# Kernel optimization log

Measured on AMD Instinct MI355X. Metric: run time of the kernel, lower is better.

Reference implementation:

```python
import jax, jax.numpy as jnp
import numpy as np

B, SQ, SK, DQ, DKV, DH, DV = 8, 2048, 2048, 1024, 1024, 1024, 1024


def setup_inputs() -> dict:
    ks = jax.random.split(jax.random.key(0), 10)
    q = jax.random.normal(ks[0], (B, SQ, DQ), dtype=jnp.float32)
    k = jax.random.normal(ks[1], (B, SK, DKV), dtype=jnp.float32)
    v = jax.random.normal(ks[2], (B, SK, DKV), dtype=jnp.float32)
    mask = jax.random.randint(ks[3], (B, SK), 0, 2).astype(jnp.bool_)
    s = 1.0 / np.sqrt(DQ)
    Wq = jax.random.normal(ks[4], (DQ, DH), dtype=jnp.float32) * s
    bq = jnp.zeros((DH,), dtype=jnp.float32)
    Wk = jax.random.normal(ks[5], (DKV, DH), dtype=jnp.float32) * s
    bk = jnp.zeros((DH,), dtype=jnp.float32)
    Wv = jax.random.normal(ks[6], (DKV, DV), dtype=jnp.float32) * s
    bv = jnp.zeros((DV,), dtype=jnp.float32)
    return {"q": q, "k": k, "v": v, "mask": mask,
            "Wq": Wq, "bq": bq, "Wk": Wk, "bk": bk, "Wv": Wv, "bv": bv}


def reference(q, k, v, mask, Wq, bq, Wk, bk, Wv, bv):
    # Linear projections
    Qp = q @ Wq + bq                       # [B, SQ, DH]
    Kp = k @ Wk + bk                       # [B, SK, DH]
    Vp = jnp.tanh(v @ Wv + bv)             # [B, SK, DV] (value has Tanh)
    # Scores; NOTE: original adds the *bool* mask, i.e. +0/+1, not -inf masking
    qk = jnp.einsum('bqd,bkd->bqk', Qp, Kp)
    qk = qk + mask[:, None, :].astype(qk.dtype)   # broadcast of mask.unsqueeze(1)
    attn = jax.nn.softmax(qk, axis=-1)
    out = jnp.einsum('bqk,bkd->bqd', attn, Vp)    # [B, SQ, DV]
    return out
```

## Files before the change

### kernel.cpp

```cpp
#include <hip/hip_runtime.h>
#include <math.h>

#define BB 8
#define SQL 2048
#define SKL 2048
#define DD 1024

typedef __attribute__((ext_vector_type(8))) short bf16x8;
typedef __attribute__((ext_vector_type(4))) float f32x4;
typedef __attribute__((ext_vector_type(4))) unsigned short us4;
typedef unsigned short u16;

__device__ __forceinline__ u16 f2bf(float f) {
    unsigned u = __float_as_uint(f);
    u += 0x7fffu + ((u >> 16) & 1u);
    return (u16)(u >> 16);
}
__device__ __forceinline__ float bf2f(u16 h) {
    return __uint_as_float((unsigned)h << 16);
}

__global__ __launch_bounds__(256)
void split3(const float* __restrict__ in, u16* __restrict__ oh,
            u16* __restrict__ ol, long n4) {
    long i = (long)blockIdx.x * 256 + threadIdx.x;
    if (i >= n4) return;
    float4 v = ((const float4*)in)[i];
    us4 h, l;
    h.x = f2bf(v.x); l.x = f2bf(v.x - bf2f(h.x));
    h.y = f2bf(v.y); l.y = f2bf(v.y - bf2f(h.y));
    h.z = f2bf(v.z); l.z = f2bf(v.z - bf2f(h.z));
    h.w = f2bf(v.w); l.w = f2bf(v.w - bf2f(h.w));
    ((us4*)oh)[i] = h;
    ((us4*)ol)[i] = l;
}

__global__ __launch_bounds__(256)
void splitT3(const float* __restrict__ W, u16* __restrict__ WhT,
             u16* __restrict__ WlT) {
    __shared__ float t[32][33];
    const int n0 = blockIdx.x * 32, k0 = blockIdx.y * 32;
    const int tx = threadIdx.x & 31, ty = threadIdx.x >> 5;
#pragma unroll
    for (int r = 0; r < 32; r += 8)
        t[ty + r][tx] = W[(long)(k0 + ty + r) * DD + n0 + tx];
    __syncthreads();
#pragma unroll
    for (int r = 0; r < 32; r += 8) {
        float x = t[tx][ty + r];
        u16 h = f2bf(x);
        WhT[(long)(n0 + ty + r) * DD + k0 + tx] = h;
        WlT[(long)(n0 + ty + r) * DD + k0 + tx] = f2bf(x - bf2f(h));
    }
}

#define GLL(gp, lp) __builtin_amdgcn_global_load_lds( \
    (const __attribute__((address_space(1))) void*)(gp), \
    (__attribute__((address_space(3))) void*)(lp), 16, 0, 0)

__global__ __launch_bounds__(512, 2)
void gemm3(const u16* __restrict__ Ah, const u16* __restrict__ Al,
           const u16* __restrict__ Bh, const u16* __restrict__ Bl,
           int lda, int ldb, int K, long sA, long sB,
           const float* __restrict__ bias, const int* __restrict__ mask, int sM,
           float* __restrict__ Cf, u16* __restrict__ C1, u16* __restrict__ C2,
           long sC, int ldc, int mode)
{
    __shared__ u16 L[65536];

    const int z = blockIdx.z;
    const long zA = (long)z * sA, zB = (long)z * sB;
    const int tid = threadIdx.x, lane = tid & 63, wave = tid >> 6;
    const int wm = wave >> 2, wn = wave & 3;
    const int l15 = lane & 15, lq = lane >> 4;
    const long row0 = (long)blockIdx.y * 256, col0 = (long)blockIdx.x * 256;

    const int pl = tid >> 8;
    const int c = tid & 255;
    const int srow = c >> 2;
    const int qg = (c & 3) ^ ((srow >> 1) & 3);
    const u16* sAp = (pl ? Al : Ah) + zA + qg * 8;
    const u16* sBp = (pl ? Bl : Bh) + zB + qg * 8;
    int ofA[4], ofB[4];
#pragma unroll
    for (int p = 0; p < 4; p++) {
        ofA[p] = (int)((row0 + p * 64 + srow) * (long)lda);
        ofB[p] = (int)((col0 + p * 64 + srow) * (long)ldb);
    }
    const int dst = tid * 8;

#define STB(p, kk, bb) GLL(sBp + ofB[p] + (kk), L + (bb) + 16384 + (p) * 4096 + dst)
#define STA(p, kk, bb) GLL(sAp + ofA[p] + (kk), L + (bb) + (p) * 4096 + dst)

    int aoff[8], boff[4];
#pragma unroll
    for (int i = 0; i < 8; i++) {
        int r = wm * 128 + i * 16 + l15;
        aoff[i] = (r >> 6) * 4096 + (r & 63) * 32 + ((lq ^ ((r >> 1) & 3)) * 8);
    }
#pragma unroll
    for (int j = 0; j < 4; j++) {
        int r = wn * 64 + j * 16 + l15;
        boff[j] = 16384 + (r >> 6) * 4096 + (r & 63) * 32 + ((lq ^ ((r >> 1) & 3)) * 8);
    }

    f32x4 acc[8][4];
#pragma unroll
    for (int i = 0; i < 8; i++)
#pragma unroll
        for (int j = 0; j < 4; j++)
#pragma unroll
            for (int e = 0; e < 4; e++) acc[i][j][e] = 0.f;

#define PHASE(mh) do { \
    bf16x8 xh[4], xl[4], yh[4], yl[4]; \
    _Pragma("unroll") \
    for (int ii = 0; ii < 4; ii++) { \
        xh[ii] = *(const bf16x8*)(L + bo + aoff[(mh) * 4 + ii]); \
        xl[ii] = *(const bf16x8*)(L + bo + aoff[(mh) * 4 + ii] + 2048); \
    } \
    _Pragma("unroll") \
    for (int j = 0; j < 4; j++) { \
        yh[j] = *(const bf16x8*)(L + bo + boff[j]); \
        yl[j] = *(const bf16x8*)(L + bo + boff[j] + 2048); \
    } \
    __builtin_amdgcn_s_setprio(1); \
    _Pragma("unroll") \
    for (int ii = 0; ii < 4; ii++) { \
        _Pragma("unroll") \
        for (int j = 0; j < 4; j++) { \
            f32x4 t_ = acc[(mh) * 4 + ii][j]; \
            t_ = __builtin_amdgcn_mfma_f32_16x16x32_bf16(xh[ii], yh[j], t_, 0, 0, 0); \
            t_ = __builtin_amdgcn_mfma_f32_16x16x32_bf16(xh[ii], yl[j], t_, 0, 0, 0); \
            t_ = __builtin_amdgcn_mfma_f32_16x16x32_bf16(xl[ii], yh[j], t_, 0, 0, 0); \
            acc[(mh) * 4 + ii][j] = t_; \
        } \
    } \
    __builtin_amdgcn_s_setprio(0); \
} while (0)

    const int NT = K >> 5;
    STB(0, 0, 0); STB(1, 0, 0); STB(2, 0, 0); STB(3, 0, 0);
    STA(0, 0, 0); STA(2, 0, 0); STA(1, 0, 0); STA(3, 0, 0);

    for (int t = 0; t < NT; ++t) {
        const int bo = (t & 1) << 15;
        const int bn = bo ^ 32768;
        const int kn = (t + 1) << 5;
        const bool pf = (t + 1) < NT;

        asm volatile("s_waitcnt vmcnt(2)" ::: "memory");
        __builtin_amdgcn_s_barrier();
        __builtin_amdgcn_sched_barrier(0);
        if (pf) { STB(0, kn, bn); STB(1, kn, bn); STB(2, kn, bn); STB(3, kn, bn); }
        PHASE(0);

        if (pf) asm volatile("s_waitcnt vmcnt(4)" ::: "memory");
        else    asm volatile("s_waitcnt vmcnt(0)" ::: "memory");
        __builtin_amdgcn_s_barrier();
        __builtin_amdgcn_sched_barrier(0);
        if (pf) { STA(0, kn, bn); STA(2, kn, bn); STA(1, kn, bn); STA(3, kn, bn); }
        PHASE(1);
    }
#undef PHASE
#undef STA
#undef STB

    const long zc = (long)z * sC;
#pragma unroll
    for (int i = 0; i < 8; i++) {
#pragma unroll
        for (int j = 0; j < 4; j++) {
            const long col = col0 + wn * 64 + j * 16 + l15;
            const long rbase = row0 + wm * 128 + i * 16 + lq * 4;
            if (mode == 0 || mode == 3) {
                const float madd = (mode == 3) ? (float)mask[(long)z * sM + col] : 0.f;
#pragma unroll
                for (int r = 0; r < 4; r++)
                    Cf[zc + (rbase + r) * (long)ldc + col] = acc[i][j][r] + madd;
            } else if (mode == 1) {
                const float bv = bias[col];
#pragma unroll
                for (int r = 0; r < 4; r++) {
                    float val = acc[i][j][r] + bv;
                    u16 h = f2bf(val);
                    C1[zc + (rbase + r) * (long)ldc + col] = h;
                    C2[zc + (rbase + r) * (long)ldc + col] = f2bf(val - bf2f(h));
                }
            } else {
                const float bv = bias[col];
                us4 o;
                o.x = f2bf(tanhf(acc[i][j][0] + bv));
                o.y = f2bf(tanhf(acc[i][j][1] + bv));
                o.z = f2bf(tanhf(acc[i][j][2] + bv));
                o.w = f2bf(tanhf(acc[i][j][3] + bv));
                *(us4*)(C1 + zc + col * (long)ldc + rbase) = o;
            }
        }
    }
}

__global__ __launch_bounds__(256, 2)
void gemm1(const u16* __restrict__ A, const u16* __restrict__ B,
           float* __restrict__ C, int lda, int ldb, int K,
           long sA, long sB, long sC, int ldc)
{
    __shared__ u16 As[4096], Bs[4096];

    const int z = blockIdx.z;
    const long zA = (long)z * sA, zB = (long)z * sB;
    const int tid = threadIdx.x, lane = tid & 63, wave = tid >> 6;
    const int wm = (wave & 1) * 64, wn = (wave >> 1) * 64;
    const int l15 = lane & 15, lq = lane >> 4;
    const long row0 = (long)blockIdx.y * 128, col0 = (long)blockIdx.x * 128;

    long offA[2], offB[2]; int lds[2];
#pragma unroll
    for (int it = 0; it < 2; it++) {
        int c = tid + it * 256, row = c >> 2;
        int qg = (c & 3) ^ ((row >> 1) & 3);
        offA[it] = (row0 + row) * (long)lda + qg * 8;
        offB[it] = (col0 + row) * (long)ldb + qg * 8;
        lds[it] = c * 8;
    }
    int aoff[4], boff[4];
#pragma unroll
    for (int i = 0; i < 4; i++) {
        int r = wm + i * 16 + l15;
        aoff[i] = r * 32 + ((lq ^ ((r >> 1) & 3)) * 8);
    }
#pragma unroll
    for (int j = 0; j < 4; j++) {
        int r = wn + j * 16 + l15;
        boff[j] = r * 32 + ((lq ^ ((r >> 1) & 3)) * 8);
    }

    f32x4 acc[4][4];
#pragma unroll
    for (int i = 0; i < 4; i++)
#pragma unroll
        for (int j = 0; j < 4; j++)
#pragma unroll
            for (int e = 0; e < 4; e++) acc[i][j][e] = 0.f;

    for (int k0 = 0; k0 < K; k0 += 32) {
#pragma unroll
        for (int it = 0; it < 2; it++) {
            GLL(A + zA + offA[it] + k0, As + lds[it]);
            GLL(B + zB + offB[it] + k0, Bs + lds[it]);
        }
        __syncthreads();
        bf16x8 af[4], bf[4];
#pragma unroll
        for (int i = 0; i < 4; i++) af[i] = *(const bf16x8*)(As + aoff[i]);
#pragma unroll
        for (int j = 0; j < 4; j++) bf[j] = *(const bf16x8*)(Bs + boff[j]);
#pragma unroll
        for (int i = 0; i < 4; i++)
#pragma unroll
            for (int j = 0; j < 4; j++)
                acc[i][j] = __builtin_amdgcn_mfma_f32_16x16x32_bf16(af[i], bf[j], acc[i][j], 0, 0, 0);
        __syncthreads();
    }

    const long zc = (long)z * sC;
#pragma unroll
    for (int i = 0; i < 4; i++)
#pragma unroll
        for (int j = 0; j < 4; j++) {
            const long col = col0 + wn + j * 16 + l15;
            const long rbase = row0 + wm + i * 16 + lq * 4;
#pragma unroll
            for (int r = 0; r < 4; r++)
                C[zc + (rbase + r) * (long)ldc + col] = acc[i][j][r];
        }
}

__global__ __launch_bounds__(256)
void softmax_bf(float* __restrict__ S)
{
    float* p = S + (long)blockIdx.x * SKL;
    u16* po = (u16*)S + (long)blockIdx.x * 2 * SKL;
    const int tid = threadIdx.x;
    const int w = tid >> 6, lane = tid & 63;

    float4 v0 = *(float4*)(p + tid * 8);
    float4 v1 = *(float4*)(p + tid * 8 + 4);

    float m = fmaxf(fmaxf(fmaxf(v0.x, v0.y), fmaxf(v0.z, v0.w)),
                    fmaxf(fmaxf(v1.x, v1.y), fmaxf(v1.z, v1.w)));
#pragma unroll
    for (int off = 32; off; off >>= 1) m = fmaxf(m, __shfl_down(m, off));

    __shared__ float wm_[4], ws_[4];
    if (lane == 0) wm_[w] = m;
    __syncthreads();
    const float bm = fmaxf(fmaxf(wm_[0], wm_[1]), fmaxf(wm_[2], wm_[3]));

    v0.x = __expf(v0.x - bm); v0.y = __expf(v0.y - bm);
    v0.z = __expf(v0.z - bm); v0.w = __expf(v0.w - bm);
    v1.x = __expf(v1.x - bm); v1.y = __expf(v1.y - bm);
    v1.z = __expf(v1.z - bm); v1.w = __expf(v1.w - bm);

    float s = v0.x + v0.y + v0.z + v0.w + v1.x + v1.y + v1.z + v1.w;
#pragma unroll
    for (int off = 32; off; off >>= 1) s += __shfl_down(s, off);
    if (lane == 0) ws_[w] = s;
    __syncthreads();
    const float inv = 1.f / (ws_[0] + ws_[1] + ws_[2] + ws_[3]);

    us4 o0, o1;
    o0.x = f2bf(v0.x * inv); o0.y = f2bf(v0.y * inv);
    o0.z = f2bf(v0.z * inv); o0.w = f2bf(v0.w * inv);
    o1.x = f2bf(v1.x * inv); o1.y = f2bf(v1.y * inv);
    o1.z = f2bf(v1.z * inv); o1.w = f2bf(v1.w * inv);
    *(us4*)(po + tid * 8) = o0;
    *(us4*)(po + tid * 8 + 4) = o1;
}

extern "C" void kernel_launch(void* const* d_in, const int* in_sizes, int n_in,
                              void* d_out, int out_size, void* d_ws, size_t ws_size,
                              hipStream_t stream)
{
    const float* q  = (const float*)d_in[0];
    const float* k  = (const float*)d_in[1];
    const float* v  = (const float*)d_in[2];
    const int* mask = (const int*)d_in[3];
    const float* Wq = (const float*)d_in[4];
    const float* bq = (const float*)d_in[5];
    const float* Wk = (const float*)d_in[6];
    const float* bk = (const float*)d_in[7];
    const float* Wv = (const float*)d_in[8];
    const float* bv = (const float*)d_in[9];
    float* out = (float*)d_out;

    const long PZ = (long)SKL * DD;
    u16*   KpH = (u16*)d_ws;
    u16*   KpL = KpH + BB * PZ;
    u16*   Vt  = KpL + BB * PZ;
    float* S   = (float*)(Vt + BB * PZ);
    u16*   inH = (u16*)S;
    u16*   inL = inH + BB * PZ;
    u16*   WhT = inL + BB * PZ;
    u16*   WlT = WhT + (long)DD * DD;
    u16*   QpH = (u16*)d_out;
    u16*   QpL = QpH + BB * PZ;
    u16*   P   = (u16*)S;

    const dim3 b256(256), b512(512);
    const long n4 = BB * PZ / 4;
    const dim3 gSplit((unsigned)(n4 / 256));
    const dim3 gW(32, 32);
    const dim3 gProj(DD / 256, SQL / 256, BB);
    const dim3 gQK(SKL / 256, SQL / 256, BB);
    const dim3 gPV(8, 16, BB);
    const dim3 gSm(BB * SQL);

    split3<<<gSplit, b256, 0, stream>>>(q, inH, inL, n4);
    splitT3<<<gW, b256, 0, stream>>>(Wq, WhT, WlT);
    gemm3<<<gProj, b512, 0, stream>>>(inH, inL, WhT, WlT, DD, DD, DD, PZ, 0,
                                      bq, nullptr, 0, nullptr, QpH, QpL, PZ, DD, 1);
    split3<<<gSplit, b256, 0, stream>>>(k, inH, inL, n4);
    splitT3<<<gW, b256, 0, stream>>>(Wk, WhT, WlT);
    gemm3<<<gProj, b512, 0, stream>>>(inH, inL, WhT, WlT, DD, DD, DD, PZ, 0,
                                      bk, nullptr, 0, nullptr, KpH, KpL, PZ, DD, 1);
    split3<<<gSplit, b256, 0, stream>>>(v, inH, inL, n4);
    splitT3<<<gW, b256, 0, stream>>>(Wv, WhT, WlT);
    gemm3<<<gProj, b512, 0, stream>>>(inH, inL, WhT, WlT, DD, DD, DD, PZ, 0,
                                      bv, nullptr, 0, nullptr, Vt, nullptr, PZ, SKL, 2);
    gemm3<<<gQK, b512, 0, stream>>>(QpH, QpL, KpH, KpL, DD, DD, DD, PZ, PZ,
                                    nullptr, mask, SKL,
                                    S, nullptr, nullptr, (long)SQL * SKL, SKL, 3);
    softmax_bf<<<gSm, b256, 0, stream>>>(S);
    gemm1<<<gPV, b256, 0, stream>>>(P, Vt, out, 2 * SKL, SKL, SKL,
                                    (long)SQL * 2 * SKL, PZ,
                                    (long)SQL * DD, DD);
}
```

Measured before the change: 850.5 us.

## Interleave global-to-LDS prefetch with MFMA in four sub-phases per K-tile

Each 32-wide K-tile's MFMA work is split into four sub-phases of two row blocks each. Next-tile B and A loads are issued in halves between them, with barriers and waitcnts placed between sub-phases. B fragments are now loaded once per tile instead of once per half, and the last iteration is peeled out so the per-iteration prefetch condition disappears. The goal is finer overlap of memory traffic with matrix cores, at the cost of more barriers per tile.

```diff
diff --git a/kernel.cpp b/kernel.cpp
--- a/kernel.cpp
+++ b/kernel.cpp
@@ -112,57 +112,76 @@
 #pragma unroll
             for (int e = 0; e < 4; e++) acc[i][j][e] = 0.f;
 
-#define PHASE(mh) do { \
-    bf16x8 xh[4], xl[4], yh[4], yl[4]; \
+#define BAR() do { __builtin_amdgcn_s_barrier(); \
+                   __builtin_amdgcn_sched_barrier(0); } while (0)
+
+#define SPX(iA, iB, GLLCODE) do { \
+    bf16x8 xh0 = *(const bf16x8*)(L + bo + aoff[iA]); \
+    bf16x8 xl0 = *(const bf16x8*)(L + bo + aoff[iA] + 2048); \
+    bf16x8 xh1 = *(const bf16x8*)(L + bo + aoff[iB]); \
+    bf16x8 xl1 = *(const bf16x8*)(L + bo + aoff[iB] + 2048); \
+    GLLCODE \
+    __builtin_amdgcn_s_setprio(1); \
     _Pragma("unroll") \
-    for (int ii = 0; ii < 4; ii++) { \
-        xh[ii] = *(const bf16x8*)(L + bo + aoff[(mh) * 4 + ii]); \
-        xl[ii] = *(const bf16x8*)(L + bo + aoff[(mh) * 4 + ii] + 2048); \
+    for (int j = 0; j < 4; j++) { \
+        f32x4 t0 = acc[iA][j]; \
+        t0 = __builtin_amdgcn_mfma_f32_16x16x32_bf16(xh0, yh[j], t0, 0, 0, 0); \
+        t0 = __builtin_amdgcn_mfma_f32_16x16x32_bf16(xh0, yl[j], t0, 0, 0, 0); \
+        t0 = __builtin_amdgcn_mfma_f32_16x16x32_bf16(xl0, yh[j], t0, 0, 0, 0); \
+        acc[iA][j] = t0; \
+        f32x4 t1 = acc[iB][j]; \
+        t1 = __builtin_amdgcn_mfma_f32_16x16x32_bf16(xh1, yh[j], t1, 0, 0, 0); \
+        t1 = __builtin_amdgcn_mfma_f32_16x16x32_bf16(xh1, yl[j], t1, 0, 0, 0); \
+        t1 = __builtin_amdgcn_mfma_f32_16x16x32_bf16(xl1, yh[j], t1, 0, 0, 0); \
+        acc[iB][j] = t1; \
     } \
+    __builtin_amdgcn_s_setprio(0); \
+} while (0)
+
+#define TILEB(PF) do { \
+    bf16x8 yh[4], yl[4]; \
     _Pragma("unroll") \
     for (int j = 0; j < 4; j++) { \
         yh[j] = *(const bf16x8*)(L + bo + boff[j]); \
         yl[j] = *(const bf16x8*)(L + bo + boff[j] + 2048); \
     } \
-    __builtin_amdgcn_s_setprio(1); \
-    _Pragma("unroll") \
-    for (int ii = 0; ii < 4; ii++) { \
-        _Pragma("unroll") \
-        for (int j = 0; j < 4; j++) { \
-            f32x4 t_ = acc[(mh) * 4 + ii][j]; \
-            t_ = __builtin_amdgcn_mfma_f32_16x16x32_bf16(xh[ii], yh[j], t_, 0, 0, 0); \
-            t_ = __builtin_amdgcn_mfma_f32_16x16x32_bf16(xh[ii], yl[j], t_, 0, 0, 0); \
-            t_ = __builtin_amdgcn_mfma_f32_16x16x32_bf16(xl[ii], yh[j], t_, 0, 0, 0); \
-            acc[(mh) * 4 + ii][j] = t_; \
-        } \
-    } \
-    __builtin_amdgcn_s_setprio(0); \
+     \
+    SPX(0, 1, if (PF) { STB(0, kn, bn); STB(1, kn, bn); }); \
+    BAR(); \
+     \
+    SPX(2, 3, if (PF) { STB(2, kn, bn); STB(3, kn, bn); }); \
+    if (PF) asm volatile("s_waitcnt vmcnt(4)" ::: "memory"); \
+    else    asm volatile("s_waitcnt vmcnt(0)" ::: "memory"); \
+    BAR(); \
+     \
+    SPX(4, 5, if (PF) { STA(0, kn, bn); STA(2, kn, bn); }); \
+    BAR(); \
+     \
+    SPX(6, 7, if (PF) { STA(1, kn, bn); STA(3, kn, bn); }); \
+    if (PF) { asm volatile("s_waitcnt vmcnt(2)" ::: "memory"); BAR(); } \
 } while (0)
 
     const int NT = K >> 5;
     STB(0, 0, 0); STB(1, 0, 0); STB(2, 0, 0); STB(3, 0, 0);
     STA(0, 0, 0); STA(2, 0, 0); STA(1, 0, 0); STA(3, 0, 0);
-
-    for (int t = 0; t < NT; ++t) {
+    asm volatile("s_waitcnt vmcnt(2)" ::: "memory");
+    BAR();
+
+    for (int t = 0; t < NT - 1; ++t) {
         const int bo = (t & 1) << 15;
         const int bn = bo ^ 32768;
         const int kn = (t + 1) << 5;
-        const bool pf = (t + 1) < NT;
-
-        asm volatile("s_waitcnt vmcnt(2)" ::: "memory");
-        __builtin_amdgcn_s_barrier();
-        __builtin_amdgcn_sched_barrier(0);
-        if (pf) { STB(0, kn, bn); STB(1, kn, bn); STB(2, kn, bn); STB(3, kn, bn); }
-        PHASE(0);
-
-        if (pf) asm volatile("s_waitcnt vmcnt(4)" ::: "memory");
-        else    asm volatile("s_waitcnt vmcnt(0)" ::: "memory");
-        __builtin_amdgcn_s_barrier();
-        __builtin_amdgcn_sched_barrier(0);
-        if (pf) { STA(0, kn, bn); STA(2, kn, bn); STA(1, kn, bn); STA(3, kn, bn); }
-        PHASE(1);
-    }
-#undef PHASE
+        TILEB(1);
+    }
+    {
+        const int bo = ((NT - 1) & 1) << 15;
+        const int bn = bo ^ 32768; (void)bn;
+        const int kn = 0; (void)kn;
+        TILEB(0);
+    }
+#undef TILEB
+#undef SPX
+#undef BAR
 #undef STA
 #undef STB
 
```

Measured after the change: 832.2 us. -2.2%, faster.
